# Optimization experiments

Measured on AMD Instinct MI355X. Metric: run time of the kernel, lower is better.

## Reference

```python
import jax, jax.numpy as jnp
import numpy as np

MEMORY_SIZE = 32768
FEATURE_DIM = 128
BATCH = 4096


def setup_inputs() -> dict:
    key = jax.random.key(0)
    k1, k2, k3, k4 = jax.random.split(key, 4)
    memory = jax.random.normal(k1, (MEMORY_SIZE, FEATURE_DIM), dtype=jnp.float32)
    input_data = jax.random.normal(k2, (BATCH, FEATURE_DIM), dtype=jnp.float32)
    write_weights = jax.random.uniform(k3, (BATCH, MEMORY_SIZE), dtype=jnp.float32)
    query = jax.random.normal(k4, (BATCH, FEATURE_DIM), dtype=jnp.float32)
    return {"memory": memory, "input_data": input_data,
            "write_weights": write_weights, "query": query}


def reference(memory, input_data, write_weights, query):
    # ---- write(): row-normalize weights, scatter-accumulate into memory ----
    # The original python double-loop computes update[j] += w[i,j] * x[i],
    # i.e. update = w_norm.T @ x  -- a single GEMM.
    w_norm = write_weights / jnp.sum(write_weights, axis=1, keepdims=True)
    update = jnp.einsum('bm,bf->mf', w_norm, input_data)  # [M, F]
    memory_new = memory + update

    # ---- read(): softmax attention over memory slots ----
    scores = jnp.matmul(query, memory_new.T)              # [B, M]
    attention_weights = jax.nn.softmax(scores, axis=1)
    retrieved_memory = jnp.matmul(attention_weights, memory_new)  # [B, F]
    confidence_scores = jnp.max(attention_weights, axis=1)        # [B]
    return retrieved_memory, confidence_scores, memory_new
```

## Files before the change

kernel.cpp:

```cpp
#include <hip/hip_runtime.h>
#include <hip/hip_bf16.h>
#include <math.h>

#define MEMSZ 32768
#define FDIM  128
#define BATCH 4096

typedef float f32x4 __attribute__((ext_vector_type(4)));
typedef _Float16 f16x8 __attribute__((ext_vector_type(8)));
typedef short bf16x8 __attribute__((ext_vector_type(8)));
typedef unsigned short u16t;
typedef unsigned int u32t;

static __device__ __forceinline__ u16t f2h_bits(float f) {
    union { _Float16 h; u16t u; } c;
    c.h = (_Float16)f;
    return c.u;
}

#define GLDS16(gsrc, ldst) \
  __builtin_amdgcn_global_load_lds((const __attribute__((address_space(1))) void*)(gsrc), \
                                   (__attribute__((address_space(3))) void*)(ldst), 16, 0, 0)

__global__ __launch_bounds__(256) void k_rowsum(const float* __restrict__ W,
                                                float* __restrict__ inv_s) {
    const int row = blockIdx.x;
    const float4* Wr = reinterpret_cast<const float4*>(W + (size_t)row * MEMSZ);
    float acc = 0.f;
    #pragma unroll 4
    for (int i = threadIdx.x; i < MEMSZ / 4; i += 256) {
        float4 v = Wr[i];
        acc += (v.x + v.y) + (v.z + v.w);
    }
    #pragma unroll
    for (int off = 32; off > 0; off >>= 1)
        acc += __shfl_down(acc, off, 64);
    __shared__ float wsum[4];
    const int lane = threadIdx.x & 63, wid = threadIdx.x >> 6;
    if (lane == 0) wsum[wid] = acc;
    __syncthreads();
    if (threadIdx.x == 0)
        inv_s[row] = 1.0f / (wsum[0] + wsum[1] + wsum[2] + wsum[3]);
}

__global__ __launch_bounds__(256) void k_prep(const float* __restrict__ X,
                                              const float* __restrict__ inv_s,
                                              unsigned char* __restrict__ XT64) {
    __shared__ float xs[64][132];
    const int T = blockIdx.x;
    const int b0 = T * 64;
    const int tid = threadIdx.x;
    #pragma unroll
    for (int i = 0; i < 8; ++i) {
        const int idx = tid + i * 256;
        const int row = idx >> 5, c4 = idx & 31;
        const float s = inv_s[b0 + row];
        float4 v = *reinterpret_cast<const float4*>(&X[(size_t)(b0 + row) * FDIM + c4 * 4]);
        v.x *= s; v.y *= s; v.z *= s; v.w *= s;
        *reinterpret_cast<float4*>(&xs[row][c4 * 4]) = v;
    }
    __syncthreads();
    #pragma unroll
    for (int i = 0; i < 4; ++i) {
        const int L = tid + i * 256;
        const int fh = L >> 9, ff = (L >> 7) & 3, ks = (L >> 6) & 1, ln = L & 63;
        const int f = fh * 64 + ff * 16 + (ln & 15);
        const int bi = ks * 32 + (ln >> 4) * 8;
        u32t pk[4];
        #pragma unroll
        for (int h = 0; h < 4; ++h) {
            const float lo = xs[bi + 2 * h][f];
            const float hi = xs[bi + 2 * h + 1][f];
            asm("v_cvt_pk_bf16_f32 %0, %1, %2" : "=v"(pk[h]) : "v"(lo), "v"(hi));
        }
        *reinterpret_cast<uint4*>(XT64 + (size_t)T * 16384 + (size_t)L * 16) =
            make_uint4(pk[0], pk[1], pk[2], pk[3]);
    }
}

#define K2B 64
#define K2M 128
__global__ __launch_bounds__(512, 2) void k_update_mfma(
    const float* __restrict__ W, const unsigned char* __restrict__ XT64,
    const float* __restrict__ Mem, float* __restrict__ MemNew,
    u16t* __restrict__ MemH, u16t* __restrict__ MemHT)
{
    __shared__ __align__(16) unsigned char wt[3][32768];

    const int tid = threadIdx.x;
    const int lane = tid & 63, w = tid >> 6;
    const int q16 = lane & 15, g = lane >> 4;
    const int wm = w >> 1, wf = w & 1;
    const int mblk = blockIdx.x * K2M;

    f32x4 acc[2][4];
    #pragma unroll
    for (int mf = 0; mf < 2; ++mf)
        #pragma unroll
        for (int ff = 0; ff < 4; ++ff) acc[mf][ff] = (f32x4){0.f, 0.f, 0.f, 0.f};

    auto stageW = [&](int buf, int t) {
        const int b0 = t * K2B;
        #pragma unroll
        for (int c = 0; c < 4; ++c) {
            const int gi = c * 512 + tid;
            const int b = gi >> 5;
            const int wb = (gi & 31) * 16;
            const int m4 = wb ^ ((b & 8) << 3);
            GLDS16((const unsigned char*)W + (size_t)(b0 + b) * (MEMSZ * 4) + (size_t)mblk * 4 + m4,
                   &wt[buf][gi * 16]);
        }
    };
    auto loadB = [&](bf16x8 (&br)[4][2], int t) {
        const unsigned char* base = XT64 + (size_t)t * 16384 + wf * 8192 + lane * 16;
        #pragma unroll
        for (int ff = 0; ff < 4; ++ff)
            #pragma unroll
            for (int ks = 0; ks < 2; ++ks)
                br[ff][ks] = *reinterpret_cast<const bf16x8*>(base + ff * 2048 + ks * 1024);
    };
    auto compute = [&](int buf, bf16x8 (&br)[4][2]) {
        bf16x8 afr[2][2];
        const unsigned char* tb = &wt[0][0] + buf * 32768;
        const int bm4 = (wm * 32 + q16) * 4;
        #pragma unroll
        for (int mf = 0; mf < 2; ++mf) {
            #pragma unroll
            for (int ks = 0; ks < 2; ++ks) {
                float av[8];
                #pragma unroll
                for (int e = 0; e < 8; ++e)
                    av[e] = *reinterpret_cast<const float*>(
                        tb + (ks * 32 + g * 8 + e) * 512 + ((bm4 + mf * 64) ^ ((g & 1) << 6)));
                union { u32t u[4]; bf16x8 v; } cv;
                #pragma unroll
                for (int h = 0; h < 4; ++h)
                    asm("v_cvt_pk_bf16_f32 %0, %1, %2" : "=v"(cv.u[h]) : "v"(av[2 * h]), "v"(av[2 * h + 1]));
                afr[mf][ks] = cv.v;
            }
        }
        #pragma unroll
        for (int mf = 0; mf < 2; ++mf)
            #pragma unroll
            for (int ff = 0; ff < 4; ++ff)
                #pragma unroll
                for (int ks = 0; ks < 2; ++ks)
                    acc[mf][ff] = __builtin_amdgcn_mfma_f32_16x16x32_bf16(
                        afr[mf][ks], br[ff][ks], acc[mf][ff], 0, 0, 0);
    };

    bf16x8 bA[4][2], bB_[4][2];
    stageW(0, 0); stageW(1, 1); loadB(bA, 0);
    const int NT = BATCH / K2B;
    for (int t = 0; t < NT; t += 2) {
        __builtin_amdgcn_s_barrier();
        if (t + 2 < NT) stageW((t + 2) % 3, t + 2);
        if (t + 1 < NT) loadB(bB_, t + 1);
        if (t + 2 < NT)      asm volatile("s_waitcnt vmcnt(16)" ::: "memory");
        else if (t + 1 < NT) asm volatile("s_waitcnt vmcnt(12)" ::: "memory");
        else                 asm volatile("s_waitcnt vmcnt(0)"  ::: "memory");
        __builtin_amdgcn_s_barrier();
        __builtin_amdgcn_sched_barrier(0);
        compute(t % 3, bA);
        if (t + 1 < NT) {
            __builtin_amdgcn_s_barrier();
            if (t + 3 < NT) stageW((t + 3) % 3, t + 3);
            if (t + 2 < NT) loadB(bA, t + 2);
            if (t + 3 < NT)      asm volatile("s_waitcnt vmcnt(16)" ::: "memory");
            else if (t + 2 < NT) asm volatile("s_waitcnt vmcnt(12)" ::: "memory");
            else                 asm volatile("s_waitcnt vmcnt(0)"  ::: "memory");
            __builtin_amdgcn_s_barrier();
            __builtin_amdgcn_sched_barrier(0);
            compute((t + 1) % 3, bB_);
        }
    }

    #pragma unroll
    for (int mf = 0; mf < 2; ++mf) {
        #pragma unroll
        for (int ff = 0; ff < 4; ++ff) {
            const int m0 = mblk + wm * 32 + mf * 16 + g * 4;
            const int fcol = wf * 64 + ff * 16 + q16;
            ushort4 ht;
            u16t* htp = reinterpret_cast<u16t*>(&ht);
            #pragma unroll
            for (int r = 0; r < 4; ++r) {
                const size_t idx = (size_t)(m0 + r) * FDIM + fcol;
                const float v = acc[mf][ff][r] + Mem[idx];
                MemNew[idx] = v;
                const u16t hb = f2h_bits(v);
                MemH[idx] = hb;
                htp[r] = hb;
            }
            *reinterpret_cast<ushort4*>(&MemHT[(size_t)fcol * MEMSZ + m0]) = ht;
        }
    }
}

#define K2_IT 16
#define K2_MT 64
__global__ __launch_bounds__(256) void k_update_f32(const float* __restrict__ W,
                                                    const float* __restrict__ X,
                                                    const float* __restrict__ inv_s,
                                                    const float* __restrict__ Mem,
                                                    float* __restrict__ MemNew) {
    __shared__ float w_lds[2][K2_IT][K2_MT];
    __shared__ float x_lds[2][K2_IT][FDIM];
    const int j0 = blockIdx.x * K2_MT;
    const int tid = threadIdx.x;
    const int tf = tid & 15;
    const int tj = tid >> 4;

    float acc[4][8];
    #pragma unroll
    for (int a = 0; a < 4; ++a)
        #pragma unroll
        for (int b = 0; b < 8; ++b) acc[a][b] = 0.f;

    float4 pw, px0, px1;
    float ps0, ps1;
    const int wr = tid >> 4, wc4 = tid & 15;
    const int xr0 = tid >> 5, xc0 = tid & 31;
    const int xr1 = (tid + 256) >> 5, xc1 = tid & 31;

    auto load_tile = [&](int it) {
        const int i0 = it * K2_IT;
        pw  = *reinterpret_cast<const float4*>(&W[(size_t)(i0 + wr) * MEMSZ + j0 + wc4 * 4]);
        px0 = *reinterpret_cast<const float4*>(&X[(size_t)(i0 + xr0) * FDIM + xc0 * 4]);
        ps0 = inv_s[i0 + xr0];
        px1 = *reinterpret_cast<const float4*>(&X[(size_t)(i0 + xr1) * FDIM + xc1 * 4]);
        ps1 = inv_s[i0 + xr1];
    };
    auto write_tile = [&](int buf) {
        *reinterpret_cast<float4*>(&w_lds[buf][wr][wc4 * 4]) = pw;
        float4 v = px0; v.x *= ps0; v.y *= ps0; v.z *= ps0; v.w *= ps0;
        *reinterpret_cast<float4*>(&x_lds[buf][xr0][xc0 * 4]) = v;
        float4 u = px1; u.x *= ps1; u.y *= ps1; u.z *= ps1; u.w *= ps1;
        *reinterpret_cast<float4*>(&x_lds[buf][xr1][xc1 * 4]) = u;
    };

    load_tile(0);
    write_tile(0);
    __syncthreads();
    const int NT = BATCH / K2_IT;
    for (int it = 0; it < NT; ++it) {
        const int cur = it & 1;
        if (it + 1 < NT) load_tile(it + 1);
        #pragma unroll 4
        for (int i = 0; i < K2_IT; ++i) {
            const float4 wv = *reinterpret_cast<const float4*>(&w_lds[cur][i][tj * 4]);
            const float4 xa = *reinterpret_cast<const float4*>(&x_lds[cur][i][tf * 4]);
            const float4 xb = *reinterpret_cast<const float4*>(&x_lds[cur][i][tf * 4 + 64]);
            const float wj[4] = {wv.x, wv.y, wv.z, wv.w};
            #pragma unroll
            for (int a = 0; a < 4; ++a) {
                acc[a][0] += wj[a] * xa.x; acc[a][1] += wj[a] * xa.y;
                acc[a][2] += wj[a] * xa.z; acc[a][3] += wj[a] * xa.w;
                acc[a][4] += wj[a] * xb.x; acc[a][5] += wj[a] * xb.y;
                acc[a][6] += wj[a] * xb.z; acc[a][7] += wj[a] * xb.w;
            }
        }
        if (it + 1 < NT) write_tile(cur ^ 1);
        __syncthreads();
    }
    #pragma unroll
    for (int a = 0; a < 4; ++a) {
        const size_t j = (size_t)j0 + tj * 4 + a;
        const float4 m0 = *reinterpret_cast<const float4*>(&Mem[j * FDIM + tf * 4]);
        const float4 m1 = *reinterpret_cast<const float4*>(&Mem[j * FDIM + tf * 4 + 64]);
        float4 o0 = {acc[a][0] + m0.x, acc[a][1] + m0.y, acc[a][2] + m0.z, acc[a][3] + m0.w};
        float4 o1 = {acc[a][4] + m1.x, acc[a][5] + m1.y, acc[a][6] + m1.z, acc[a][7] + m1.w};
        *reinterpret_cast<float4*>(&MemNew[j * FDIM + tf * 4]) = o0;
        *reinterpret_cast<float4*>(&MemNew[j * FDIM + tf * 4 + 64]) = o1;
    }
}

__global__ __launch_bounds__(256) void k_attn_mfma(
    const float* __restrict__ Q, const u16t* __restrict__ Kh, const u16t* __restrict__ KhT,
    float* __restrict__ accP, float* __restrict__ mP, float* __restrict__ lP, int s_shift)
{
    __shared__ __align__(16) unsigned char kv_u8[2][16384];
    __shared__ __align__(16) unsigned char v_u8[2][16384];
    __shared__ __align__(16) unsigned char p_u8[4][2048];

    const int tid = threadIdx.x;
    const int w = tid >> 6, lane = tid & 63;
    const int q16 = lane & 15, g = lane >> 4;
    const int S = 1 << s_shift;
    const int s_idx = blockIdx.x & (S - 1);
    const int qb = blockIdx.x >> s_shift;
    const int chunk = MEMSZ >> s_shift;
    const int slot0 = s_idx * chunk;
    const int NT = chunk >> 6;

    f16x8 qfrag[2][4];
    #pragma unroll
    for (int qf = 0; qf < 2; ++qf) {
        const float* qrow = Q + (size_t)(qb * 128 + w * 32 + qf * 16 + q16) * FDIM;
        #pragma unroll
        for (int ks = 0; ks < 4; ++ks) {
            float tmp[8];
            *reinterpret_cast<float4*>(&tmp[0]) = *reinterpret_cast<const float4*>(&qrow[ks * 32 + g * 8]);
            *reinterpret_cast<float4*>(&tmp[4]) = *reinterpret_cast<const float4*>(&qrow[ks * 32 + g * 8 + 4]);
            f16x8 v;
            #pragma unroll
            for (int e = 0; e < 8; ++e) v[e] = (_Float16)tmp[e];
            qfrag[qf][ks] = v;
        }
    }

    auto stage = [&](int buf, int tile) {
        const unsigned char* kbase = (const unsigned char*)Kh + (size_t)(slot0 + tile * 64) * 256;
        const unsigned char* tbase = (const unsigned char*)KhT + (size_t)(slot0 + tile * 64) * 2;
        #pragma unroll
        for (int c = 0; c < 4; ++c) {
            const int C = w * 4 + c;
            const int pp = C * 1024 + lane * 16;
            {
                const int slot = pp >> 8;
                const int inner = (pp & 255) ^ ((slot & 7) << 4);
                GLDS16(kbase + slot * 256 + inner, &kv_u8[buf][C * 1024]);
            }
            {
                const int d = pp >> 7;
                const int inner = (pp & 127) ^ ((d & 7) << 4);
                GLDS16(tbase + (size_t)d * 65536 + inner, &v_u8[buf][C * 1024]);
            }
        }
    };

    float m_run[2] = {-3.0e38f, -3.0e38f};
    float l_run[2] = {0.f, 0.f};
    f32x4 acc_o[8][2];
    #pragma unroll
    for (int df = 0; df < 8; ++df)
        #pragma unroll
        for (int qf = 0; qf < 2; ++qf)
            acc_o[df][qf] = (f32x4){0.f, 0.f, 0.f, 0.f};

    stage(0, 0);
    asm volatile("s_waitcnt vmcnt(0)" ::: "memory");
    __builtin_amdgcn_s_barrier();
    __builtin_amdgcn_sched_barrier(0);

    int cur = 0;
    for (int t = 0; t < NT; ++t) {
        if (t + 1 < NT) stage(cur ^ 1, t + 1);

        f32x4 acc_s[4][2];
        #pragma unroll
        for (int sf = 0; sf < 4; ++sf) {
            acc_s[sf][0] = (f32x4){0.f, 0.f, 0.f, 0.f};
            acc_s[sf][1] = (f32x4){0.f, 0.f, 0.f, 0.f};
        }
        const unsigned char* kvb = &kv_u8[cur][0];
        #pragma unroll
        for (int ks = 0; ks < 4; ++ks) {
            #pragma unroll
            for (int sf = 0; sf < 4; ++sf) {
                const int slot = sf * 16 + q16;
                const f16x8 a = *reinterpret_cast<const f16x8*>(
                    kvb + slot * 256 + ((ks * 64 + g * 16) ^ ((slot & 7) << 4)));
                acc_s[sf][0] = __builtin_amdgcn_mfma_f32_16x16x32_f16(a, qfrag[0][ks], acc_s[sf][0], 0, 0, 0);
                acc_s[sf][1] = __builtin_amdgcn_mfma_f32_16x16x32_f16(a, qfrag[1][ks], acc_s[sf][1], 0, 0, 0);
            }
        }

        f16x8 pb[2][2];
        unsigned char* pw = &p_u8[w][0];
        #pragma unroll
        for (int qf = 0; qf < 2; ++qf) {
            float pmax = acc_s[0][qf][0];
            #pragma unroll
            for (int sf = 0; sf < 4; ++sf)
                #pragma unroll
                for (int r = 0; r < 4; ++r)
                    pmax = fmaxf(pmax, acc_s[sf][qf][r]);
            pmax = fmaxf(pmax, __shfl_xor(pmax, 16));
            pmax = fmaxf(pmax, __shfl_xor(pmax, 32));
            const float mn = fmaxf(m_run[qf], pmax);
            float p[4][4];
            float psum = 0.f;
            #pragma unroll
            for (int sf = 0; sf < 4; ++sf)
                #pragma unroll
                for (int r = 0; r < 4; ++r) {
                    p[sf][r] = __expf(acc_s[sf][qf][r] - mn);
                    psum += p[sf][r];
                }
            psum += __shfl_xor(psum, 16);
            psum += __shfl_xor(psum, 32);
            const float sc = __expf(m_run[qf] - mn);
            l_run[qf] = l_run[qf] * sc + psum;
            m_run[qf] = mn;
            #pragma unroll
            for (int df = 0; df < 8; ++df) {
                acc_o[df][qf][0] *= sc; acc_o[df][qf][1] *= sc;
                acc_o[df][qf][2] *= sc; acc_o[df][qf][3] *= sc;
            }
            #pragma unroll
            for (int sf = 0; sf < 4; ++sf)
                #pragma unroll
                for (int rr = 0; rr < 2; ++rr) {
                    const u32t val = (u32t)f2h_bits(p[sf][2 * rr]) | ((u32t)f2h_bits(p[sf][2 * rr + 1]) << 16);
                    const int byte = q16 * 128 + (((sf * 16 + g * 4 + 2 * rr) * 2) ^ ((q16 & 7) << 4));
                    *reinterpret_cast<u32t*>(pw + byte) = val;
                }
            #pragma unroll
            for (int kk = 0; kk < 2; ++kk) {
                const int byte = q16 * 128 + (((kk * 32 + g * 8) * 2) ^ ((q16 & 7) << 4));
                pb[qf][kk] = *reinterpret_cast<const f16x8*>(pw + byte);
            }
        }

        const unsigned char* vb = &v_u8[cur][0];
        #pragma unroll
        for (int df = 0; df < 8; ++df) {
            #pragma unroll
            for (int kk = 0; kk < 2; ++kk) {
                const int d = df * 16 + q16;
                const f16x8 av = *reinterpret_cast<const f16x8*>(
                    vb + d * 128 + ((kk * 64 + g * 16) ^ ((d & 7) << 4)));
                acc_o[df][0] = __builtin_amdgcn_mfma_f32_16x16x32_f16(av, pb[0][kk], acc_o[df][0], 0, 0, 0);
                acc_o[df][1] = __builtin_amdgcn_mfma_f32_16x16x32_f16(av, pb[1][kk], acc_o[df][1], 0, 0, 0);
            }
        }

        asm volatile("s_waitcnt vmcnt(0)" ::: "memory");
        __builtin_amdgcn_s_barrier();
        __builtin_amdgcn_sched_barrier(0);
        cur ^= 1;
    }

    const int rowbase = qb * 128 + w * 32;
    #pragma unroll
    for (int qf = 0; qf < 2; ++qf) {
        const int row = rowbase + qf * 16 + q16;
        float* ap = accP + ((size_t)s_idx * BATCH + row) * FDIM;
        #pragma unroll
        for (int df = 0; df < 8; ++df) {
            float4 o = {acc_o[df][qf][0], acc_o[df][qf][1], acc_o[df][qf][2], acc_o[df][qf][3]};
            *reinterpret_cast<float4*>(&ap[df * 16 + g * 4]) = o;
        }
        if (g == 0) {
            mP[(size_t)s_idx * BATCH + row] = m_run[qf];
            lP[(size_t)s_idx * BATCH + row] = l_run[qf];
        }
    }
}

__global__ __launch_bounds__(256) void k_combine(const float* __restrict__ mP,
                                                 const float* __restrict__ lP,
                                                 const float* __restrict__ accP,
                                                 float* __restrict__ Out,
                                                 float* __restrict__ Conf, int S) {
    const int row = blockIdx.x * 8 + (threadIdx.x >> 5);
    const int lane = threadIdx.x & 31;
    float mt = -3.0e38f;
    for (int s = 0; s < S; ++s) mt = fmaxf(mt, mP[(size_t)s * BATCH + row]);
    float lt = 0.f;
    for (int s = 0; s < S; ++s) lt += lP[(size_t)s * BATCH + row] * __expf(mP[(size_t)s * BATCH + row] - mt);
    const float inv = 1.0f / lt;
    float4 o = {0.f, 0.f, 0.f, 0.f};
    for (int s = 0; s < S; ++s) {
        const float wgt = __expf(mP[(size_t)s * BATCH + row] - mt);
        const float4 a = *reinterpret_cast<const float4*>(&accP[((size_t)s * BATCH + row) * FDIM + lane * 4]);
        o.x += wgt * a.x; o.y += wgt * a.y; o.z += wgt * a.z; o.w += wgt * a.w;
    }
    float4 res = {o.x * inv, o.y * inv, o.z * inv, o.w * inv};
    *reinterpret_cast<float4*>(&Out[(size_t)row * FDIM + lane * 4]) = res;
    if (lane == 0) Conf[row] = inv;
}

#define QT 16
#define MT 64
#define LSTR (FDIM + 4)
__global__ __launch_bounds__(256) void k_attn_f32(const float* __restrict__ Q,
                                                  const float* __restrict__ MemNew,
                                                  float* __restrict__ Out,
                                                  float* __restrict__ Conf) {
    __shared__ float mem_lds[MT][LSTR];
    __shared__ float q_lds[QT][LSTR];
    __shared__ float p_lds[QT][MT];
    __shared__ float m_lds[QT], l_lds[QT], scale_lds[QT];

    const int tid = threadIdx.x;
    const int qblk = blockIdx.x * QT;

    #pragma unroll
    for (int r = 0; r < 2; ++r) {
        const int idx = tid + r * 256;
        const int row = idx >> 5, c4 = idx & 31;
        *reinterpret_cast<float4*>(&q_lds[row][c4 * 4]) =
            *reinterpret_cast<const float4*>(&Q[(size_t)(qblk + row) * FDIM + c4 * 4]);
    }
    if (tid < QT) { m_lds[tid] = -3.0e38f; l_lds[tid] = 0.f; }

    const int sq = (tid >> 5) * 2;
    const int sm = tid & 31;
    const int pq = tid >> 4;
    const int pf = (tid & 15) * 4;

    float acc[8];
    #pragma unroll
    for (int e = 0; e < 8; ++e) acc[e] = 0.f;

    for (int mt = 0; mt < MEMSZ / MT; ++mt) {
        __syncthreads();
        const float* src = MemNew + (size_t)mt * MT * FDIM;
        #pragma unroll
        for (int r = 0; r < 8; ++r) {
            const int idx = tid + r * 256;
            const int row = idx >> 5, c4 = idx & 31;
            *reinterpret_cast<float4*>(&mem_lds[row][c4 * 4]) =
                *reinterpret_cast<const float4*>(&src[(size_t)row * FDIM + c4 * 4]);
        }
        const float mold0 = m_lds[sq], mold1 = m_lds[sq + 1];
        __syncthreads();

        float s00 = 0.f, s01 = 0.f, s10 = 0.f, s11 = 0.f;
        #pragma unroll 8
        for (int k = 0; k < FDIM; k += 4) {
            const float4 qa = *reinterpret_cast<const float4*>(&q_lds[sq][k]);
            const float4 qb = *reinterpret_cast<const float4*>(&q_lds[sq + 1][k]);
            const float4 ma = *reinterpret_cast<const float4*>(&mem_lds[sm][k]);
            const float4 mb = *reinterpret_cast<const float4*>(&mem_lds[sm + 32][k]);
            s00 += qa.x*ma.x + qa.y*ma.y + qa.z*ma.z + qa.w*ma.w;
            s01 += qa.x*mb.x + qa.y*mb.y + qa.z*mb.z + qa.w*mb.w;
            s10 += qb.x*ma.x + qb.y*ma.y + qb.z*ma.z + qb.w*ma.w;
            s11 += qb.x*mb.x + qb.y*mb.y + qb.z*mb.z + qb.w*mb.w;
        }
        float r0 = fmaxf(s00, s01), r1 = fmaxf(s10, s11);
        #pragma unroll
        for (int off = 1; off <= 16; off <<= 1) {
            r0 = fmaxf(r0, __shfl_xor(r0, off, 64));
            r1 = fmaxf(r1, __shfl_xor(r1, off, 64));
        }
        const float mn0 = fmaxf(mold0, r0), mn1 = fmaxf(mold1, r1);
        const float p00 = __expf(s00 - mn0), p01 = __expf(s01 - mn0);
        const float p10 = __expf(s10 - mn1), p11 = __expf(s11 - mn1);
        float t0 = p00 + p01, t1 = p10 + p11;
        #pragma unroll
        for (int off = 1; off <= 16; off <<= 1) {
            t0 += __shfl_xor(t0, off, 64);
            t1 += __shfl_xor(t1, off, 64);
        }
        p_lds[sq][sm]      = p00; p_lds[sq][sm + 32]     = p01;
        p_lds[sq + 1][sm]  = p10; p_lds[sq + 1][sm + 32] = p11;
        if (sm == 0) {
            const float sc0 = __expf(mold0 - mn0), sc1 = __expf(mold1 - mn1);
            m_lds[sq] = mn0; m_lds[sq + 1] = mn1;
            l_lds[sq]     = l_lds[sq]     * sc0 + t0;
            l_lds[sq + 1] = l_lds[sq + 1] * sc1 + t1;
            scale_lds[sq] = sc0; scale_lds[sq + 1] = sc1;
        }
        __syncthreads();

        const float sc = scale_lds[pq];
        #pragma unroll
        for (int e = 0; e < 8; ++e) acc[e] *= sc;
        #pragma unroll 8
        for (int m = 0; m < MT; ++m) {
            const float p = p_lds[pq][m];
            const float4 va = *reinterpret_cast<const float4*>(&mem_lds[m][pf]);
            const float4 vb = *reinterpret_cast<const float4*>(&mem_lds[m][pf + 64]);
            acc[0] += p * va.x; acc[1] += p * va.y; acc[2] += p * va.z; acc[3] += p * va.w;
            acc[4] += p * vb.x; acc[5] += p * vb.y; acc[6] += p * vb.z; acc[7] += p * vb.w;
        }
    }
    const float linv = 1.0f / l_lds[pq];
    float4 o0 = {acc[0]*linv, acc[1]*linv, acc[2]*linv, acc[3]*linv};
    float4 o1 = {acc[4]*linv, acc[5]*linv, acc[6]*linv, acc[7]*linv};
    *reinterpret_cast<float4*>(&Out[(size_t)(qblk + pq) * FDIM + pf]) = o0;
    *reinterpret_cast<float4*>(&Out[(size_t)(qblk + pq) * FDIM + pf + 64]) = o1;
    if (tid < QT) Conf[qblk + tid] = 1.0f / l_lds[tid];
}

extern "C" void kernel_launch(void* const* d_in, const int* in_sizes, int n_in,
                              void* d_out, int out_size, void* d_ws, size_t ws_size,
                              hipStream_t stream) {
    (void)in_sizes; (void)n_in; (void)out_size;
    const float* memory   = (const float*)d_in[0];
    const float* input    = (const float*)d_in[1];
    const float* wweights = (const float*)d_in[2];
    const float* query    = (const float*)d_in[3];

    float* out       = (float*)d_out;
    float* retrieved = out;
    float* conf      = out + (size_t)BATCH * FDIM;
    float* mem_new   = conf + BATCH;

    char* ws = (char*)d_ws;
    float* inv_s = (float*)ws;
    const size_t off_xt   = 16384;
    const size_t off_h    = off_xt + (size_t)FDIM * BATCH * 2;
    const size_t off_hT   = off_h + (size_t)MEMSZ * FDIM * 2;
    const size_t off_part = off_hT + (size_t)MEMSZ * FDIM * 2;

    int s_shift = -1;
    for (int sh = 4; sh >= 0; --sh) {
        const size_t S = (size_t)1 << sh;
        const size_t need = off_part + S * ((size_t)BATCH * 8 + (size_t)BATCH * FDIM * 4);
        if (ws_size >= need) { s_shift = sh; break; }
    }

    k_rowsum<<<BATCH, 256, 0, stream>>>(wweights, inv_s);
    if (s_shift >= 0) {
        const int S = 1 << s_shift;
        unsigned char* xt64 = (unsigned char*)(ws + off_xt);
        u16t* mh  = (u16t*)(ws + off_h);
        u16t* mhT = (u16t*)(ws + off_hT);
        float* mP   = (float*)(ws + off_part);
        float* lP   = mP + (size_t)S * BATCH;
        float* accP = lP + (size_t)S * BATCH;
        k_prep<<<BATCH / 64, 256, 0, stream>>>(input, inv_s, xt64);
        k_update_mfma<<<MEMSZ / K2M, 512, 0, stream>>>(wweights, xt64, memory, mem_new, mh, mhT);
        k_attn_mfma<<<(BATCH / 128) * S, 256, 0, stream>>>(query, mh, mhT, accP, mP, lP, s_shift);
        k_combine<<<BATCH / 8, 256, 0, stream>>>(mP, lP, accP, retrieved, conf, S);
    } else {
        k_update_f32<<<MEMSZ / K2_MT, 256, 0, stream>>>(wweights, input, inv_s, memory, mem_new);
        k_attn_f32<<<BATCH / QT, 256, 0, stream>>>(query, mem_new, retrieved, conf);
    }
}
```

Measured before the change: 407.7 us.

## Fuse row-sum with bf16 pre-transpose of write weights; stream bf16 tiles into MFMA update

A new kernel reads each 64x128 tile of the fp32 write-weight matrix once. It computes partial row sums and writes a bf16 copy already laid out in MFMA fragment order. A small kernel then reduces the partial sums into inverse row sums. The update GEMM loads ready-made bf16 A fragments straight from global memory into registers with double buffering, which drops the LDS staging, barriers and in-loop fp32-to-bf16 conversion. The cost is a 256 MB bf16 intermediate written and re-read, and a larger workspace requirement; if the workspace is too small, the code falls back to the slow fp32 path.

```diff
diff --git a/kernel.cpp b/kernel.cpp
--- a/kernel.cpp
+++ b/kernel.cpp
@@ -22,25 +22,70 @@
   __builtin_amdgcn_global_load_lds((const __attribute__((address_space(1))) void*)(gsrc), \
                                    (__attribute__((address_space(3))) void*)(ldst), 16, 0, 0)
 
-__global__ __launch_bounds__(256) void k_rowsum(const float* __restrict__ W,
-                                                float* __restrict__ inv_s) {
-    const int row = blockIdx.x;
-    const float4* Wr = reinterpret_cast<const float4*>(W + (size_t)row * MEMSZ);
-    float acc = 0.f;
-    #pragma unroll 4
-    for (int i = threadIdx.x; i < MEMSZ / 4; i += 256) {
-        float4 v = Wr[i];
-        acc += (v.x + v.y) + (v.z + v.w);
-    }
-    #pragma unroll
-    for (int off = 32; off > 0; off >>= 1)
-        acc += __shfl_down(acc, off, 64);
-    __shared__ float wsum[4];
-    const int lane = threadIdx.x & 63, wid = threadIdx.x >> 6;
-    if (lane == 0) wsum[wid] = acc;
+__global__ __launch_bounds__(256) void k_sumT(const float* __restrict__ W,
+                                              float* __restrict__ partial,
+                                              unsigned char* __restrict__ WT64) {
+    __shared__ __align__(16) unsigned char xs[32768];
+    const int tid = threadIdx.x;
+    const int bt = blockIdx.x & 63, mt = blockIdx.x >> 6;
+
+    #pragma unroll
+    for (int i = 0; i < 8; ++i) {
+        const int gi = tid + i * 256;
+        const int b = gi >> 5;
+        const int srcoff = ((gi & 31) * 16) ^ ((b & 7) << 4);
+        GLDS16((const unsigned char*)W + ((size_t)(bt * 64 + b) * MEMSZ + (size_t)mt * 128) * 4 + srcoff,
+               &xs[gi * 16]);
+    }
+    asm volatile("s_waitcnt vmcnt(0)" ::: "memory");
     __syncthreads();
-    if (threadIdx.x == 0)
-        inv_s[row] = 1.0f / (wsum[0] + wsum[1] + wsum[2] + wsum[3]);
+
+    {
+        const int b = tid >> 2, q = tid & 3;
+        float s = 0.f;
+        #pragma unroll
+        for (int j = 0; j < 8; ++j) {
+            const int off = b * 512 + ((q * 128 + j * 16) ^ ((b & 7) << 4));
+            const float4 v = *reinterpret_cast<const float4*>(&xs[off]);
+            s += (v.x + v.y) + (v.z + v.w);
+        }
+        s += __shfl_xor(s, 1);
+        s += __shfl_xor(s, 2);
+        if (q == 0) partial[(size_t)mt * BATCH + bt * 64 + b] = s;
+    }
+
+    unsigned char* dst = WT64 + ((size_t)mt * 64 + bt) * 16384;
+    #pragma unroll
+    for (int k = 0; k < 4; ++k) {
+        const int ci = tid + k * 256;
+        const int wm = ci >> 8, mf = (ci >> 7) & 1, ks = (ci >> 6) & 1;
+        const int l6 = ci & 63, g = l6 >> 4, q16 = l6 & 15;
+        const int m = wm * 32 + mf * 16 + q16;
+        u32t pk[4];
+        #pragma unroll
+        for (int h = 0; h < 4; ++h) {
+            const int b0 = ks * 32 + g * 8 + 2 * h;
+            const float lo = *reinterpret_cast<const float*>(
+                &xs[b0 * 512 + ((m * 4) ^ ((b0 & 7) << 4))]);
+            const float hi = *reinterpret_cast<const float*>(
+                &xs[(b0 + 1) * 512 + ((m * 4) ^ (((b0 + 1) & 7) << 4))]);
+            asm("v_cvt_pk_bf16_f32 %0, %1, %2" : "=v"(pk[h]) : "v"(lo), "v"(hi));
+        }
+        *reinterpret_cast<uint4*>(dst + ci * 16) = make_uint4(pk[0], pk[1], pk[2], pk[3]);
+    }
+}
+
+__global__ __launch_bounds__(256) void k_inv(const float* __restrict__ partial,
+                                             float* __restrict__ inv_s) {
+    const int b = blockIdx.x * 256 + threadIdx.x;
+    float s0 = 0.f, s1 = 0.f, s2 = 0.f, s3 = 0.f;
+    for (int mt = 0; mt < 256; mt += 4) {
+        s0 += partial[(size_t)mt * BATCH + b];
+        s1 += partial[(size_t)(mt + 1) * BATCH + b];
+        s2 += partial[(size_t)(mt + 2) * BATCH + b];
+        s3 += partial[(size_t)(mt + 3) * BATCH + b];
+    }
+    inv_s[b] = 1.0f / ((s0 + s1) + (s2 + s3));
 }
 
 __global__ __launch_bounds__(256) void k_prep(const float* __restrict__ X,
@@ -78,20 +123,20 @@
     }
 }
 
-#define K2B 64
-#define K2M 128
-__global__ __launch_bounds__(512, 2) void k_update_mfma(
-    const float* __restrict__ W, const unsigned char* __restrict__ XT64,
+__global__ __launch_bounds__(512, 2) void k_update_mfma2(
+    const unsigned char* __restrict__ WT64, const unsigned char* __restrict__ XT64,
     const float* __restrict__ Mem, float* __restrict__ MemNew,
     u16t* __restrict__ MemH, u16t* __restrict__ MemHT)
 {
-    __shared__ __align__(16) unsigned char wt[3][32768];
-
     const int tid = threadIdx.x;
     const int lane = tid & 63, w = tid >> 6;
     const int q16 = lane & 15, g = lane >> 4;
     const int wm = w >> 1, wf = w & 1;
-    const int mblk = blockIdx.x * K2M;
+    const int mblk = blockIdx.x * 128;
+
+    const unsigned char* wbase = WT64 + (size_t)blockIdx.x * (64 * 16384)
+                               + (size_t)(wm * 4096 + lane * 16);
+    const unsigned char* xbase = XT64 + (size_t)(wf * 8192 + lane * 16);
 
     f32x4 acc[2][4];
     #pragma unroll
@@ -99,46 +144,21 @@
         #pragma unroll
         for (int ff = 0; ff < 4; ++ff) acc[mf][ff] = (f32x4){0.f, 0.f, 0.f, 0.f};
 
-    auto stageW = [&](int buf, int t) {
-        const int b0 = t * K2B;
-        #pragma unroll
-        for (int c = 0; c < 4; ++c) {
-            const int gi = c * 512 + tid;
-            const int b = gi >> 5;
-            const int wb = (gi & 31) * 16;
-            const int m4 = wb ^ ((b & 8) << 3);
-            GLDS16((const unsigned char*)W + (size_t)(b0 + b) * (MEMSZ * 4) + (size_t)mblk * 4 + m4,
-                   &wt[buf][gi * 16]);
-        }
+    auto issue = [&](bf16x8 (&ar)[2][2], bf16x8 (&br)[4][2], int t) {
+        const unsigned char* wp = wbase + (size_t)t * 16384;
+        #pragma unroll
+        for (int mf = 0; mf < 2; ++mf)
+            #pragma unroll
+            for (int ks = 0; ks < 2; ++ks)
+                ar[mf][ks] = *reinterpret_cast<const bf16x8*>(wp + mf * 2048 + ks * 1024);
+        const unsigned char* xp = xbase + (size_t)t * 16384;
+        #pragma unroll
+        for (int ff = 0; ff < 4; ++ff)
+            #pragma unroll
+            for (int ks = 0; ks < 2; ++ks)
+                br[ff][ks] = *reinterpret_cast<const bf16x8*>(xp + ff * 2048 + ks * 1024);
     };
-    auto loadB = [&](bf16x8 (&br)[4][2], int t) {
-        const unsigned char* base = XT64 + (size_t)t * 16384 + wf * 8192 + lane * 16;
-        #pragma unroll
-        for (int ff = 0; ff < 4; ++ff)
-            #pragma unroll
-            for (int ks = 0; ks < 2; ++ks)
-                br[ff][ks] = *reinterpret_cast<const bf16x8*>(base + ff * 2048 + ks * 1024);
-    };
-    auto compute = [&](int buf, bf16x8 (&br)[4][2]) {
-        bf16x8 afr[2][2];
-        const unsigned char* tb = &wt[0][0] + buf * 32768;
-        const int bm4 = (wm * 32 + q16) * 4;
-        #pragma unroll
-        for (int mf = 0; mf < 2; ++mf) {
-            #pragma unroll
-            for (int ks = 0; ks < 2; ++ks) {
-                float av[8];
-                #pragma unroll
-                for (int e = 0; e < 8; ++e)
-                    av[e] = *reinterpret_cast<const float*>(
-                        tb + (ks * 32 + g * 8 + e) * 512 + ((bm4 + mf * 64) ^ ((g & 1) << 6)));
-                union { u32t u[4]; bf16x8 v; } cv;
-                #pragma unroll
-                for (int h = 0; h < 4; ++h)
-                    asm("v_cvt_pk_bf16_f32 %0, %1, %2" : "=v"(cv.u[h]) : "v"(av[2 * h]), "v"(av[2 * h + 1]));
-                afr[mf][ks] = cv.v;
-            }
-        }
+    auto compute = [&](bf16x8 (&ar)[2][2], bf16x8 (&br)[4][2]) {
         #pragma unroll
         for (int mf = 0; mf < 2; ++mf)
             #pragma unroll
@@ -146,33 +166,17 @@
                 #pragma unroll
                 for (int ks = 0; ks < 2; ++ks)
                     acc[mf][ff] = __builtin_amdgcn_mfma_f32_16x16x32_bf16(
-                        afr[mf][ks], br[ff][ks], acc[mf][ff], 0, 0, 0);
+                        ar[mf][ks], br[ff][ks], acc[mf][ff], 0, 0, 0);
     };
 
-    bf16x8 bA[4][2], bB_[4][2];
-    stageW(0, 0); stageW(1, 1); loadB(bA, 0);
-    const int NT = BATCH / K2B;
+    bf16x8 aE[2][2], bE[4][2], aO[2][2], bO[4][2];
+    issue(aE, bE, 0); issue(aO, bO, 1);
+    const int NT = BATCH / 64;
     for (int t = 0; t < NT; t += 2) {
-        __builtin_amdgcn_s_barrier();
-        if (t + 2 < NT) stageW((t + 2) % 3, t + 2);
-        if (t + 1 < NT) loadB(bB_, t + 1);
-        if (t + 2 < NT)      asm volatile("s_waitcnt vmcnt(16)" ::: "memory");
-        else if (t + 1 < NT) asm volatile("s_waitcnt vmcnt(12)" ::: "memory");
-        else                 asm volatile("s_waitcnt vmcnt(0)"  ::: "memory");
-        __builtin_amdgcn_s_barrier();
-        __builtin_amdgcn_sched_barrier(0);
-        compute(t % 3, bA);
-        if (t + 1 < NT) {
-            __builtin_amdgcn_s_barrier();
-            if (t + 3 < NT) stageW((t + 3) % 3, t + 3);
-            if (t + 2 < NT) loadB(bA, t + 2);
-            if (t + 3 < NT)      asm volatile("s_waitcnt vmcnt(16)" ::: "memory");
-            else if (t + 2 < NT) asm volatile("s_waitcnt vmcnt(12)" ::: "memory");
-            else                 asm volatile("s_waitcnt vmcnt(0)"  ::: "memory");
-            __builtin_amdgcn_s_barrier();
-            __builtin_amdgcn_sched_barrier(0);
-            compute((t + 1) % 3, bB_);
-        }
+        compute(aE, bE);
+        if (t + 2 < NT) issue(aE, bE, t + 2);
+        compute(aO, bO);
+        if (t + 3 < NT) issue(aO, bO, t + 3);
     }
 
     #pragma unroll
@@ -194,84 +198,6 @@
             }
             *reinterpret_cast<ushort4*>(&MemHT[(size_t)fcol * MEMSZ + m0]) = ht;
         }
-    }
-}
-
-#define K2_IT 16
-#define K2_MT 64
-__global__ __launch_bounds__(256) void k_update_f32(const float* __restrict__ W,
-                                                    const float* __restrict__ X,
-                                                    const float* __restrict__ inv_s,
-                                                    const float* __restrict__ Mem,
-                                                    float* __restrict__ MemNew) {
-    __shared__ float w_lds[2][K2_IT][K2_MT];
-    __shared__ float x_lds[2][K2_IT][FDIM];
-    const int j0 = blockIdx.x * K2_MT;
-    const int tid = threadIdx.x;
-    const int tf = tid & 15;
-    const int tj = tid >> 4;
-
-    float acc[4][8];
-    #pragma unroll
-    for (int a = 0; a < 4; ++a)
-        #pragma unroll
-        for (int b = 0; b < 8; ++b) acc[a][b] = 0.f;
-
-    float4 pw, px0, px1;
-    float ps0, ps1;
-    const int wr = tid >> 4, wc4 = tid & 15;
-    const int xr0 = tid >> 5, xc0 = tid & 31;
-    const int xr1 = (tid + 256) >> 5, xc1 = tid & 31;
-
-    auto load_tile = [&](int it) {
-        const int i0 = it * K2_IT;
-        pw  = *reinterpret_cast<const float4*>(&W[(size_t)(i0 + wr) * MEMSZ + j0 + wc4 * 4]);
-        px0 = *reinterpret_cast<const float4*>(&X[(size_t)(i0 + xr0) * FDIM + xc0 * 4]);
-        ps0 = inv_s[i0 + xr0];
-        px1 = *reinterpret_cast<const float4*>(&X[(size_t)(i0 + xr1) * FDIM + xc1 * 4]);
-        ps1 = inv_s[i0 + xr1];
-    };
-    auto write_tile = [&](int buf) {
-        *reinterpret_cast<float4*>(&w_lds[buf][wr][wc4 * 4]) = pw;
-        float4 v = px0; v.x *= ps0; v.y *= ps0; v.z *= ps0; v.w *= ps0;
-        *reinterpret_cast<float4*>(&x_lds[buf][xr0][xc0 * 4]) = v;
-        float4 u = px1; u.x *= ps1; u.y *= ps1; u.z *= ps1; u.w *= ps1;
-        *reinterpret_cast<float4*>(&x_lds[buf][xr1][xc1 * 4]) = u;
-    };
-
-    load_tile(0);
-    write_tile(0);
-    __syncthreads();
-    const int NT = BATCH / K2_IT;
-    for (int it = 0; it < NT; ++it) {
-        const int cur = it & 1;
-        if (it + 1 < NT) load_tile(it + 1);
-        #pragma unroll 4
-        for (int i = 0; i < K2_IT; ++i) {
-            const float4 wv = *reinterpret_cast<const float4*>(&w_lds[cur][i][tj * 4]);
-            const float4 xa = *reinterpret_cast<const float4*>(&x_lds[cur][i][tf * 4]);
-            const float4 xb = *reinterpret_cast<const float4*>(&x_lds[cur][i][tf * 4 + 64]);
-            const float wj[4] = {wv.x, wv.y, wv.z, wv.w};
-            #pragma unroll
-            for (int a = 0; a < 4; ++a) {
-                acc[a][0] += wj[a] * xa.x; acc[a][1] += wj[a] * xa.y;
-                acc[a][2] += wj[a] * xa.z; acc[a][3] += wj[a] * xa.w;
-                acc[a][4] += wj[a] * xb.x; acc[a][5] += wj[a] * xb.y;
-                acc[a][6] += wj[a] * xb.z; acc[a][7] += wj[a] * xb.w;
-            }
-        }
-        if (it + 1 < NT) write_tile(cur ^ 1);
-        __syncthreads();
-    }
-    #pragma unroll
-    for (int a = 0; a < 4; ++a) {
-        const size_t j = (size_t)j0 + tj * 4 + a;
-        const float4 m0 = *reinterpret_cast<const float4*>(&Mem[j * FDIM + tf * 4]);
-        const float4 m1 = *reinterpret_cast<const float4*>(&Mem[j * FDIM + tf * 4 + 64]);
-        float4 o0 = {acc[a][0] + m0.x, acc[a][1] + m0.y, acc[a][2] + m0.z, acc[a][3] + m0.w};
-        float4 o1 = {acc[a][4] + m1.x, acc[a][5] + m1.y, acc[a][6] + m1.z, acc[a][7] + m1.w};
-        *reinterpret_cast<float4*>(&MemNew[j * FDIM + tf * 4]) = o0;
-        *reinterpret_cast<float4*>(&MemNew[j * FDIM + tf * 4 + 64]) = o1;
     }
 }
 
@@ -472,6 +398,105 @@
     if (lane == 0) Conf[row] = inv;
 }
 
+__global__ __launch_bounds__(256) void k_rowsum(const float* __restrict__ W,
+                                                float* __restrict__ inv_s) {
+    const int row = blockIdx.x;
+    const float4* Wr = reinterpret_cast<const float4*>(W + (size_t)row * MEMSZ);
+    float acc = 0.f;
+    #pragma unroll 4
+    for (int i = threadIdx.x; i < MEMSZ / 4; i += 256) {
+        float4 v = Wr[i];
+        acc += (v.x + v.y) + (v.z + v.w);
+    }
+    #pragma unroll
+    for (int off = 32; off > 0; off >>= 1)
+        acc += __shfl_down(acc, off, 64);
+    __shared__ float wsum[4];
+    const int lane = threadIdx.x & 63, wid = threadIdx.x >> 6;
+    if (lane == 0) wsum[wid] = acc;
+    __syncthreads();
+    if (threadIdx.x == 0)
+        inv_s[row] = 1.0f / (wsum[0] + wsum[1] + wsum[2] + wsum[3]);
+}
+
+#define K2_IT 16
+#define K2_MT 64
+__global__ __launch_bounds__(256) void k_update_f32(const float* __restrict__ W,
+                                                    const float* __restrict__ X,
+                                                    const float* __restrict__ inv_s,
+                                                    const float* __restrict__ Mem,
+                                                    float* __restrict__ MemNew) {
+    __shared__ float w_lds[2][K2_IT][K2_MT];
+    __shared__ float x_lds[2][K2_IT][FDIM];
+    const int j0 = blockIdx.x * K2_MT;
+    const int tid = threadIdx.x;
+    const int tf = tid & 15;
+    const int tj = tid >> 4;
+
+    float acc[4][8];
+    #pragma unroll
+    for (int a = 0; a < 4; ++a)
+        #pragma unroll
+        for (int b = 0; b < 8; ++b) acc[a][b] = 0.f;
+
+    float4 pw, px0, px1;
+    float ps0, ps1;
+    const int wr = tid >> 4, wc4 = tid & 15;
+    const int xr0 = tid >> 5, xc0 = tid & 31;
+    const int xr1 = (tid + 256) >> 5, xc1 = tid & 31;
+
+    auto load_tile = [&](int it) {
+        const int i0 = it * K2_IT;
+        pw  = *reinterpret_cast<const float4*>(&W[(size_t)(i0 + wr) * MEMSZ + j0 + wc4 * 4]);
+        px0 = *reinterpret_cast<const float4*>(&X[(size_t)(i0 + xr0) * FDIM + xc0 * 4]);
+        ps0 = inv_s[i0 + xr0];
+        px1 = *reinterpret_cast<const float4*>(&X[(size_t)(i0 + xr1) * FDIM + xc1 * 4]);
+        ps1 = inv_s[i0 + xr1];
+    };
+    auto write_tile = [&](int buf) {
+        *reinterpret_cast<float4*>(&w_lds[buf][wr][wc4 * 4]) = pw;
+        float4 v = px0; v.x *= ps0; v.y *= ps0; v.z *= ps0; v.w *= ps0;
+        *reinterpret_cast<float4*>(&x_lds[buf][xr0][xc0 * 4]) = v;
+        float4 u = px1; u.x *= ps1; u.y *= ps1; u.z *= ps1; u.w *= ps1;
+        *reinterpret_cast<float4*>(&x_lds[buf][xr1][xc1 * 4]) = u;
+    };
+
+    load_tile(0);
+    write_tile(0);
+    __syncthreads();
+    const int NT = BATCH / K2_IT;
+    for (int it = 0; it < NT; ++it) {
+        const int cur = it & 1;
+        if (it + 1 < NT) load_tile(it + 1);
+        #pragma unroll 4
+        for (int i = 0; i < K2_IT; ++i) {
+            const float4 wv = *reinterpret_cast<const float4*>(&w_lds[cur][i][tj * 4]);
+            const float4 xa = *reinterpret_cast<const float4*>(&x_lds[cur][i][tf * 4]);
+            const float4 xb = *reinterpret_cast<const float4*>(&x_lds[cur][i][tf * 4 + 64]);
+            const float wj[4] = {wv.x, wv.y, wv.z, wv.w};
+            #pragma unroll
+            for (int a = 0; a < 4; ++a) {
+                acc[a][0] += wj[a] * xa.x; acc[a][1] += wj[a] * xa.y;
+                acc[a][2] += wj[a] * xa.z; acc[a][3] += wj[a] * xa.w;
+                acc[a][4] += wj[a] * xb.x; acc[a][5] += wj[a] * xb.y;
+                acc[a][6] += wj[a] * xb.z; acc[a][7] += wj[a] * xb.w;
+            }
+        }
+        if (it + 1 < NT) write_tile(cur ^ 1);
+        __syncthreads();
+    }
+    #pragma unroll
+    for (int a = 0; a < 4; ++a) {
+        const size_t j = (size_t)j0 + tj * 4 + a;
+        const float4 m0 = *reinterpret_cast<const float4*>(&Mem[j * FDIM + tf * 4]);
+        const float4 m1 = *reinterpret_cast<const float4*>(&Mem[j * FDIM + tf * 4 + 64]);
+        float4 o0 = {acc[a][0] + m0.x, acc[a][1] + m0.y, acc[a][2] + m0.z, acc[a][3] + m0.w};
+        float4 o1 = {acc[a][4] + m1.x, acc[a][5] + m1.y, acc[a][6] + m1.z, acc[a][7] + m1.w};
+        *reinterpret_cast<float4*>(&MemNew[j * FDIM + tf * 4]) = o0;
+        *reinterpret_cast<float4*>(&MemNew[j * FDIM + tf * 4 + 64]) = o1;
+    }
+}
+
 #define QT 16
 #define MT 64
 #define LSTR (FDIM + 4)
@@ -592,32 +617,34 @@
 
     char* ws = (char*)d_ws;
     float* inv_s = (float*)ws;
+
     const size_t off_xt   = 16384;
-    const size_t off_h    = off_xt + (size_t)FDIM * BATCH * 2;
-    const size_t off_hT   = off_h + (size_t)MEMSZ * FDIM * 2;
-    const size_t off_part = off_hT + (size_t)MEMSZ * FDIM * 2;
-
-    int s_shift = -1;
-    for (int sh = 4; sh >= 0; --sh) {
-        const size_t S = (size_t)1 << sh;
-        const size_t need = off_part + S * ((size_t)BATCH * 8 + (size_t)BATCH * FDIM * 4);
-        if (ws_size >= need) { s_shift = sh; break; }
-    }
-
-    k_rowsum<<<BATCH, 256, 0, stream>>>(wweights, inv_s);
-    if (s_shift >= 0) {
-        const int S = 1 << s_shift;
+    const size_t off_part = off_xt + ((size_t)FDIM * BATCH * 2);
+    const size_t off_h    = off_part + ((size_t)256 * BATCH * 4);
+    const size_t off_hT   = off_h + ((size_t)MEMSZ * FDIM * 2);
+    const size_t off_pc   = off_hT + ((size_t)MEMSZ * FDIM * 2);
+    const size_t sz_pc    = (size_t)16 * ((size_t)BATCH * 8 + (size_t)BATCH * FDIM * 4);
+    const size_t off_wt   = off_pc + sz_pc;
+    const size_t need     = off_wt + (size_t)64 * 256 * 16384;
+
+    if (ws_size >= need) {
         unsigned char* xt64 = (unsigned char*)(ws + off_xt);
-        u16t* mh  = (u16t*)(ws + off_h);
-        u16t* mhT = (u16t*)(ws + off_hT);
-        float* mP   = (float*)(ws + off_part);
-        float* lP   = mP + (size_t)S * BATCH;
-        float* accP = lP + (size_t)S * BATCH;
+        float* part = (float*)(ws + off_part);
+        u16t* mh    = (u16t*)(ws + off_h);
+        u16t* mhT   = (u16t*)(ws + off_hT);
+        float* mP   = (float*)(ws + off_pc);
+        float* lP   = mP + (size_t)16 * BATCH;
+        float* accP = lP + (size_t)16 * BATCH;
+        unsigned char* wt64 = (unsigned char*)(ws + off_wt);
+
+        k_sumT<<<64 * 256, 256, 0, stream>>>(wweights, part, wt64);
+        k_inv<<<BATCH / 256, 256, 0, stream>>>(part, inv_s);
         k_prep<<<BATCH / 64, 256, 0, stream>>>(input, inv_s, xt64);
-        k_update_mfma<<<MEMSZ / K2M, 512, 0, stream>>>(wweights, xt64, memory, mem_new, mh, mhT);
-        k_attn_mfma<<<(BATCH / 128) * S, 256, 0, stream>>>(query, mh, mhT, accP, mP, lP, s_shift);
-        k_combine<<<BATCH / 8, 256, 0, stream>>>(mP, lP, accP, retrieved, conf, S);
+        k_update_mfma2<<<MEMSZ / 128, 512, 0, stream>>>(wt64, xt64, memory, mem_new, mh, mhT);
+        k_attn_mfma<<<(BATCH / 128) * 16, 256, 0, stream>>>(query, mh, mhT, accP, mP, lP, 4);
+        k_combine<<<BATCH / 8, 256, 0, stream>>>(mP, lP, accP, retrieved, conf, 16);
     } else {
+        k_rowsum<<<BATCH, 256, 0, stream>>>(wweights, inv_s);
         k_update_f32<<<MEMSZ / K2_MT, 256, 0, stream>>>(wweights, input, inv_s, memory, mem_new);
         k_attn_f32<<<BATCH / QT, 256, 0, stream>>>(query, mem_new, retrieved, conf);
     }
```

New measurement: 478.4 us. 1.17x slower.

## Halve update-kernel M tile to 64 with 256 threads and double-buffered LDS

Applied to the files above, without the earlier changes.

The weight-transpose GEMM now uses a 64-row memory tile per block with 256 threads instead of 128 rows with 512 threads, doubling the grid. The LDS staging for W drops from a three-deep to a two-deep ring of 16KB buffers, with a matching XOR swizzle and a prefetch distance of one tile. The aim is more resident blocks per CU and better latency hiding for the large streaming read of write_weights. In exchange, prefetch depth is shallower and each block reuses the XT tiles over fewer memory rows.

```diff
diff --git a/kernel.cpp b/kernel.cpp
--- a/kernel.cpp
+++ b/kernel.cpp
@@ -79,13 +79,13 @@
 }
 
 #define K2B 64
-#define K2M 128
-__global__ __launch_bounds__(512, 2) void k_update_mfma(
+#define K2M 64
+__global__ __launch_bounds__(256, 2) void k_update_mfma(
     const float* __restrict__ W, const unsigned char* __restrict__ XT64,
     const float* __restrict__ Mem, float* __restrict__ MemNew,
     u16t* __restrict__ MemH, u16t* __restrict__ MemHT)
 {
-    __shared__ __align__(16) unsigned char wt[3][32768];
+    __shared__ __align__(16) unsigned char wt[2][16384];
 
     const int tid = threadIdx.x;
     const int lane = tid & 63, w = tid >> 6;
@@ -99,39 +99,42 @@
         #pragma unroll
         for (int ff = 0; ff < 4; ++ff) acc[mf][ff] = (f32x4){0.f, 0.f, 0.f, 0.f};
 
+    const unsigned char* xbase = XT64 + (size_t)(wf * 8192 + lane * 16);
+
     auto stageW = [&](int buf, int t) {
         const int b0 = t * K2B;
         #pragma unroll
         for (int c = 0; c < 4; ++c) {
-            const int gi = c * 512 + tid;
-            const int b = gi >> 5;
-            const int wb = (gi & 31) * 16;
-            const int m4 = wb ^ ((b & 8) << 3);
-            GLDS16((const unsigned char*)W + (size_t)(b0 + b) * (MEMSZ * 4) + (size_t)mblk * 4 + m4,
+            const int gi = c * 256 + tid;
+            const int b = gi >> 4;
+            const int src = ((gi & 15) * 16) ^ ((b & 8) << 1);
+            GLDS16((const unsigned char*)W + (size_t)(b0 + b) * (MEMSZ * 4) + (size_t)mblk * 4 + src,
                    &wt[buf][gi * 16]);
         }
     };
     auto loadB = [&](bf16x8 (&br)[4][2], int t) {
-        const unsigned char* base = XT64 + (size_t)t * 16384 + wf * 8192 + lane * 16;
+        const unsigned char* xp = xbase + (size_t)t * 16384;
         #pragma unroll
         for (int ff = 0; ff < 4; ++ff)
             #pragma unroll
             for (int ks = 0; ks < 2; ++ks)
-                br[ff][ks] = *reinterpret_cast<const bf16x8*>(base + ff * 2048 + ks * 1024);
+                br[ff][ks] = *reinterpret_cast<const bf16x8*>(xp + ff * 2048 + ks * 1024);
     };
     auto compute = [&](int buf, bf16x8 (&br)[4][2]) {
         bf16x8 afr[2][2];
-        const unsigned char* tb = &wt[0][0] + buf * 32768;
-        const int bm4 = (wm * 32 + q16) * 4;
+        const unsigned char* tb = &wt[buf][0];
         #pragma unroll
         for (int mf = 0; mf < 2; ++mf) {
+            const int mm4 = (wm * 32 + mf * 16 + q16) * 4;
             #pragma unroll
             for (int ks = 0; ks < 2; ++ks) {
                 float av[8];
                 #pragma unroll
-                for (int e = 0; e < 8; ++e)
+                for (int e = 0; e < 8; ++e) {
+                    const int b = ks * 32 + g * 8 + e;
                     av[e] = *reinterpret_cast<const float*>(
-                        tb + (ks * 32 + g * 8 + e) * 512 + ((bm4 + mf * 64) ^ ((g & 1) << 6)));
+                        tb + b * 256 + (mm4 ^ ((b & 8) << 1)));
+                }
                 union { u32t u[4]; bf16x8 v; } cv;
                 #pragma unroll
                 for (int h = 0; h < 4; ++h)
@@ -150,29 +153,23 @@
     };
 
     bf16x8 bA[4][2], bB_[4][2];
-    stageW(0, 0); stageW(1, 1); loadB(bA, 0);
+    stageW(0, 0); loadB(bA, 0);
     const int NT = BATCH / K2B;
     for (int t = 0; t < NT; t += 2) {
         __builtin_amdgcn_s_barrier();
-        if (t + 2 < NT) stageW((t + 2) % 3, t + 2);
-        if (t + 1 < NT) loadB(bB_, t + 1);
-        if (t + 2 < NT)      asm volatile("s_waitcnt vmcnt(16)" ::: "memory");
-        else if (t + 1 < NT) asm volatile("s_waitcnt vmcnt(12)" ::: "memory");
-        else                 asm volatile("s_waitcnt vmcnt(0)"  ::: "memory");
+        if (t + 1 < NT) { loadB(bB_, t + 1); stageW(1, t + 1); }
+        if (t + 1 < NT) asm volatile("s_waitcnt vmcnt(12)" ::: "memory");
+        else            asm volatile("s_waitcnt vmcnt(0)"  ::: "memory");
         __builtin_amdgcn_s_barrier();
         __builtin_amdgcn_sched_barrier(0);
-        compute(t % 3, bA);
-        if (t + 1 < NT) {
-            __builtin_amdgcn_s_barrier();
-            if (t + 3 < NT) stageW((t + 3) % 3, t + 3);
-            if (t + 2 < NT) loadB(bA, t + 2);
-            if (t + 3 < NT)      asm volatile("s_waitcnt vmcnt(16)" ::: "memory");
-            else if (t + 2 < NT) asm volatile("s_waitcnt vmcnt(12)" ::: "memory");
-            else                 asm volatile("s_waitcnt vmcnt(0)"  ::: "memory");
-            __builtin_amdgcn_s_barrier();
-            __builtin_amdgcn_sched_barrier(0);
-            compute((t + 1) % 3, bB_);
-        }
+        compute(0, bA);
+        __builtin_amdgcn_s_barrier();
+        if (t + 2 < NT) { loadB(bA, t + 2); stageW(0, t + 2); }
+        if (t + 2 < NT) asm volatile("s_waitcnt vmcnt(12)" ::: "memory");
+        else            asm volatile("s_waitcnt vmcnt(0)"  ::: "memory");
+        __builtin_amdgcn_s_barrier();
+        __builtin_amdgcn_sched_barrier(0);
+        compute(1, bB_);
     }
 
     #pragma unroll
@@ -614,7 +611,7 @@
         float* lP   = mP + (size_t)S * BATCH;
         float* accP = lP + (size_t)S * BATCH;
         k_prep<<<BATCH / 64, 256, 0, stream>>>(input, inv_s, xt64);
-        k_update_mfma<<<MEMSZ / K2M, 512, 0, stream>>>(wweights, xt64, memory, mem_new, mh, mhT);
+        k_update_mfma<<<MEMSZ / K2M, 256, 0, stream>>>(wweights, xt64, memory, mem_new, mh, mhT);
         k_attn_mfma<<<(BATCH / 128) * S, 256, 0, stream>>>(query, mh, mhT, accP, mP, lP, s_shift);
         k_combine<<<BATCH / 8, 256, 0, stream>>>(mP, lP, accP, retrieved, conf, S);
     } else {
```

After: 399.3 us. -2.1%, faster.
